# Optimization experiments

Measured on AMD Instinct MI355X. Metric: run time of the kernel, lower is better.

## Reference

```python
import jax, jax.numpy as jnp
import numpy as np

B, L, D = 16, 512, 128
EPS = 1e-12


def _newton_schulz_1(S):
    # One Newton-Schulz orthogonalization iteration on batched [B,D,D] matrices:
    # X = S/||S||_F ; X <- 1.5*X - 0.5 * X @ X^T @ X
    norm = jnp.sqrt(jnp.sum(S * S, axis=(-2, -1), keepdims=True)) + 1e-6
    X = S / norm
    XXtX = jnp.einsum('bij,bkj,bkl->bil', X, X, X)
    return 1.5 * X - 0.5 * XXtX


def _poly(v, coeffs):
    # PolynomialFeatureLayer, degree 2, dimension-preserving:
    # phi(v) = c0*v + c1*v^2
    return coeffs[0] * v + coeffs[1] * v * v


def setup_inputs() -> dict:
    key = jax.random.key(0)
    ks = jax.random.split(key, 6)
    s = 1.0 / np.sqrt(D)
    x = jax.random.normal(ks[0], (B, L, D), jnp.float32)
    Wq = jax.random.normal(ks[1], (D, D), jnp.float32) * s
    Wk = jax.random.normal(ks[2], (D, D), jnp.float32) * s
    Wout = jax.random.normal(ks[3], (D, D), jnp.float32) * s
    bout = jnp.zeros((D,), jnp.float32)
    M0 = jax.random.normal(ks[4], (D, D), jnp.float32) * 0.01   # M_init
    S0 = jnp.zeros((D, D), jnp.float32)                          # S_init
    P0 = jnp.eye(D, dtype=jnp.float32) * 0.01                    # P_init
    log_gain = jnp.zeros((D,), jnp.float32)                      # QKProjectionLayer gain
    coeffs = jnp.array([1.0, 0.5], jnp.float32)                  # poly coeffs
    return {"x": x, "Wq": Wq, "Wk": Wk, "P0": P0, "M0": M0, "S0": S0,
            "log_gain": log_gain, "coeffs": coeffs, "Wout": Wout, "bout": bout}


def reference(x, Wq, Wk, P0, M0, S0, log_gain, coeffs, Wout, bout):
    b, l, d = x.shape
    q = jnp.einsum('bld,ed->ble', x, Wq)                 # q_proj (no bias)
    k = jnp.einsum('bld,ed->ble', x, Wk)                 # k_proj (no bias)
    k = k / jnp.maximum(jnp.linalg.norm(k, axis=-1, keepdims=True), EPS)  # F.normalize

    # QKProjectionLayer: rotate q by per-batch projection P, tanh gate with learned gain
    P = jnp.broadcast_to(P0, (b, d, d))
    gain = jnp.exp(log_gain)
    q_aligned = jnp.tanh(gain * jnp.einsum('bld,bde->ble', q, P))
    # (P_new = 0.99*P + 0.01*mean_t outer(q,k); state only, unused by output)

    k_phi = _poly(k, coeffs)
    q_phi = _poly(q_aligned, coeffs)

    M = jnp.broadcast_to(M0, (b, d, d))
    S = jnpp = jnp.broadcast_to(S0, (b, d, d))

    def step(carry, inputs):
        M, S = carry
        k_t, q_t, x_t = inputs                           # each [B,D]
        pred = jnp.einsum('bde,be->bd', M, k_t)
        err = pred - x_t
        S = 0.9 * S + err[:, :, None] * k_t[:, None, :]  # outer-product grad
        S_ortho = _newton_schulz_1(S)
        M = 0.99 * M - 0.01 * S_ortho
        y_t = jnp.einsum('bde,be->bd', M, q_t)
        return (M, S), y_t

    xs = (jnp.swapaxes(k_phi, 0, 1), jnp.swapaxes(q_phi, 0, 1), jnp.swapaxes(x, 0, 1))
    (_, _), ys = jax.lax.scan(step, (M, S), xs)          # ys: [L,B,D]
    stacked = jnp.swapaxes(ys, 0, 1)                     # [B,L,D]
    out = jnp.einsum('bld,ed->ble', stacked, Wout) + bout  # out_proj
    return out
```

## Files before the change

### kernel.cpp

```cpp
#include <hip/hip_runtime.h>

#define BB 16
#define LL 512
#define DD 128
#define CH 16
#define NCH (LL / CH)

typedef float v2f __attribute__((ext_vector_type(2)));
__device__ __forceinline__ v2f mk2(float x, float y) { v2f r; r.x = x; r.y = y; return r; }
__device__ __forceinline__ v2f fma2(v2f a, v2f b, v2f c) {
    return __builtin_elementwise_fma(a, b, c);
}

__device__ __forceinline__ float red8(float v) {
    v += __int_as_float(__builtin_amdgcn_update_dpp(
            0, __float_as_int(v), 0xB1, 0xF, 0xF, true));
    v += __int_as_float(__builtin_amdgcn_update_dpp(
            0, __float_as_int(v), 0x4E, 0xF, 0xF, true));
    v += __int_as_float(__builtin_amdgcn_update_dpp(
            0, __float_as_int(v), 0x141, 0xF, 0xF, true));
    return v;
}

#define SCAN_REGS __attribute__((amdgpu_waves_per_eu(2, 2)))

__global__ void transpose3_kernel(const float* __restrict__ Wq,
                                  const float* __restrict__ Wk,
                                  const float* __restrict__ Wout,
                                  float* __restrict__ WqT,
                                  float* __restrict__ WkT,
                                  float* __restrict__ WoutT) {
    const float* src; float* dst;
    if (blockIdx.x == 0)      { src = Wq;   dst = WqT;   }
    else if (blockIdx.x == 1) { src = Wk;   dst = WkT;   }
    else                      { src = Wout; dst = WoutT; }
    for (int idx = threadIdx.x; idx < DD * DD; idx += blockDim.x) {
        int r = idx >> 7, c = idx & 127;
        dst[c * DD + r] = src[idx];
    }
}

__global__ __launch_bounds__(128) void prologue_kernel(
        const float* __restrict__ x, const float* __restrict__ WqT,
        const float* __restrict__ WkT, const float* __restrict__ P0,
        const float* __restrict__ log_gain, const float* __restrict__ coeffs,
        float* __restrict__ kphi, float* __restrict__ qphi) {
    const int row0 = blockIdx.x * 8;
    const int e = threadIdx.x;
    __shared__ float xs[8][DD];
    __shared__ float qrow[8][DD];
    __shared__ float wred[8][2];

    #pragma unroll
    for (int rr = 0; rr < 8; ++rr)
        xs[rr][e] = x[(size_t)(row0 + rr) * DD + e];
    __syncthreads();

    float aq[8] = {0,0,0,0,0,0,0,0}, ak[8] = {0,0,0,0,0,0,0,0};
    #pragma unroll 4
    for (int d = 0; d < DD; ++d) {
        float wq = WqT[d * DD + e];
        float wk = WkT[d * DD + e];
        #pragma unroll
        for (int rr = 0; rr < 8; ++rr) {
            float xv = xs[rr][d];
            aq[rr] = fmaf(xv, wq, aq[rr]);
            ak[rr] = fmaf(xv, wk, ak[rr]);
        }
    }
    const int lane = threadIdx.x & 63, wv = threadIdx.x >> 6;
    #pragma unroll
    for (int rr = 0; rr < 8; ++rr) {
        float s = ak[rr] * ak[rr];
        #pragma unroll
        for (int m = 1; m <= 32; m <<= 1) s += __shfl_xor(s, m);
        if (lane == 0) wred[rr][wv] = s;
    }
    __syncthreads();
    const float c0 = coeffs[0], c1v = coeffs[1];
    #pragma unroll
    for (int rr = 0; rr < 8; ++rr) {
        float s = wred[rr][0] + wred[rr][1];
        float kn = ak[rr] / fmaxf(sqrtf(s), 1e-12f);
        kphi[(size_t)(row0 + rr) * DD + e] = c0 * kn + c1v * kn * kn;
        qrow[rr][e] = aq[rr];
    }
    __syncthreads();
    float acc[8] = {0,0,0,0,0,0,0,0};
    #pragma unroll 4
    for (int d = 0; d < DD; ++d) {
        float pv = P0[d * DD + e];
        #pragma unroll
        for (int rr = 0; rr < 8; ++rr) acc[rr] = fmaf(qrow[rr][d], pv, acc[rr]);
    }
    const float g = expf(log_gain[e]);
    #pragma unroll
    for (int rr = 0; rr < 8; ++rr) {
        float qa = tanhf(g * acc[rr]);
        qphi[(size_t)(row0 + rr) * DD + e] = c0 * qa + c1v * qa * qa;
    }
}

__global__ SCAN_REGS __launch_bounds__(512)
void scan_kernel(
        const float* __restrict__ kphi, const float* __restrict__ qphi,
        const float* __restrict__ x, const float* __restrict__ M0,
        const float* __restrict__ S0, float* __restrict__ ys) {
    const int b    = blockIdx.x;
    const int tid  = threadIdx.x;
    const int j    = tid & 7;
    const int g    = tid >> 3;
    const int r0   = 2 * g;
    const int w    = tid >> 6;
    const int lane = tid & 63;

    __shared__ __align__(16) float kc[2][CH * DD];
    __shared__ __align__(16) float qc[2][CH * DD];
    __shared__ __align__(16) float xc[2][CH * DD];
    __shared__ __align__(16) float yc[CH * DD];
    __shared__ __align__(16) float us[DD], ps[DD], wsv[DD], hs[DD];
    __shared__ float red[64];
    __shared__ float n2sh;

    v2f S2[16], ST2[16], A2[16], M2[16];
    {
        const float4* S04 = (const float4*)S0;
        const float4* M04 = (const float4*)M0;
        #pragma unroll
        for (int rl = 0; rl < 2; ++rl)
            #pragma unroll
            for (int m = 0; m < 4; ++m) {
                int f4 = (r0 + rl) * 32 + j + 8 * m;
                float4 s4 = S04[f4], m4 = M04[f4];
                int p = rl * 8 + 2 * m;
                S2[p]     = mk2(s4.x, s4.y);
                S2[p + 1] = mk2(s4.z, s4.w);
                M2[p]     = mk2(m4.x, m4.y);
                M2[p + 1] = mk2(m4.z, m4.w);
            }
        #pragma unroll
        for (int rl = 0; rl < 2; ++rl)
            #pragma unroll
            for (int m = 0; m < 4; ++m) {
                int p = rl * 8 + 2 * m;
                ST2[p]     = mk2(S0[(size_t)(4*j + 32*m + 0) * DD + r0 + rl],
                                 S0[(size_t)(4*j + 32*m + 1) * DD + r0 + rl]);
                ST2[p + 1] = mk2(S0[(size_t)(4*j + 32*m + 2) * DD + r0 + rl],
                                 S0[(size_t)(4*j + 32*m + 3) * DD + r0 + rl]);
            }
        #pragma unroll
        for (int p = 0; p < 16; ++p) A2[p] = mk2(0.f, 0.f);
    }

    float sp = 0.f;
    #pragma unroll
    for (int p = 0; p < 16; ++p) {
        sp = fmaf(S2[p].x, S2[p].x, sp);
        sp = fmaf(S2[p].y, S2[p].y, sp);
    }
    sp = red8(sp);
    if (j == 0) red[g] = sp;

    const size_t base = (size_t)b * LL * DD;

    #pragma unroll
    for (int i = 0; i < 3; ++i) {
        int seg = w * 3 + i, arr = seg >> 3, sub = seg & 7;
        const float* sp0 = (arr == 0 ? kphi : (arr == 1 ? qphi : x))
                           + base + sub * 256 + lane * 4;
        float* dp = (arr == 0 ? kc[0] : (arr == 1 ? qc[0] : xc[0]))
                    + sub * 256 + lane * 4;
        *(float4*)dp = *(const float4*)sp0;
    }
    __syncthreads();
    if (tid < 64) {
        float s = red[tid];
        #pragma unroll
        for (int m = 1; m <= 32; m <<= 1) s += __shfl_xor(s, m);
        if (tid == 0) n2sh = s;
    }
    __syncthreads();
    float n2 = n2sh;

    const float a = 0.9f, a2v = 0.81f, a3v = 0.729f;
    const v2f av = mk2(a, a);

    v2f kk2[8];
    float u0, u1, p0, p1, cv;
    {
        const float4* k4 = (const float4*)kc[0];
        v2f pr0v = mk2(0.f, 0.f), pr1v = mk2(0.f, 0.f);
        v2f pp0v = mk2(0.f, 0.f), pp1v = mk2(0.f, 0.f);
        v2f cvv  = mk2(0.f, 0.f);
        #pragma unroll
        for (int m = 0; m < 4; ++m) {
            float4 v4 = k4[j + 8 * m];
            v2f k0 = mk2(v4.x, v4.y), k1 = mk2(v4.z, v4.w);
            kk2[2*m] = k0; kk2[2*m + 1] = k1;
            pr0v = fma2(M2[2*m],     k0, pr0v);
            pr0v = fma2(M2[2*m + 1], k1, pr0v);
            pr1v = fma2(M2[8 + 2*m],     k0, pr1v);
            pr1v = fma2(M2[8 + 2*m + 1], k1, pr1v);
            pp0v = fma2(S2[2*m],     k0, pp0v);
            pp0v = fma2(S2[2*m + 1], k1, pp0v);
            pp1v = fma2(S2[8 + 2*m],     k0, pp1v);
            pp1v = fma2(S2[8 + 2*m + 1], k1, pp1v);
            cvv  = fma2(k0, k0, cvv);
            cvv  = fma2(k1, k1, cvv);
        }
        float pr0 = red8(pr0v.x + pr0v.y);
        float pr1 = red8(pr1v.x + pr1v.y);
        p0 = red8(pp0v.x + pp0v.y);
        p1 = red8(pp1v.x + pp1v.y);
        cv = red8(cvv.x + cvv.y);
        const float2 xv = *(const float2*)&xc[0][r0];
        u0 = pr0 - xv.x; u1 = pr1 - xv.y;
        if (j == 0) {
            *(float2*)&us[r0] = make_float2(u0, u1);
            *(float2*)&ps[r0] = make_float2(p0, p1);
        }
    }
    __syncthreads();

    #pragma unroll 1
    for (int tc = 0; tc < NCH; ++tc) {
        const int cb = tc & 1;
        const float* kcb = kc[cb];
        const float* qcb = qc[cb];
        const float* xcb = xc[cb];

        #pragma unroll 1
        for (int sl = 0; sl < CH; ++sl) {
            const int so = sl * DD;
            const bool last = (tc == NCH - 1) && (sl == CH - 1);

            float4 pre0, pre1, pre2;
            const bool doPre = (sl == 0) && (tc + 1 < NCH);
            if (doPre) {
                const size_t nbg = base + (size_t)(tc + 1) * CH * DD;
                {
                    int seg = w * 3 + 0, arr = seg >> 3, sub = seg & 7;
                    pre0 = *(const float4*)((arr == 0 ? kphi : (arr == 1 ? qphi : x))
                                            + nbg + sub * 256 + lane * 4);
                }
                {
                    int seg = w * 3 + 1, arr = seg >> 3, sub = seg & 7;
                    pre1 = *(const float4*)((arr == 0 ? kphi : (arr == 1 ? qphi : x))
                                            + nbg + sub * 256 + lane * 4);
                }
                {
                    int seg = w * 3 + 2, arr = seg >> 3, sub = seg & 7;
                    pre2 = *(const float4*)((arr == 0 ? kphi : (arr == 1 ? qphi : x))
                                            + nbg + sub * 256 + lane * 4);
                }
            }

            v2f uu2[8], pa2[8];
            {
                const float4* u4 = (const float4*)us;
                const float4* p4 = (const float4*)ps;
                #pragma unroll
                for (int m = 0; m < 4; ++m) {
                    float4 a4 = u4[j + 8 * m], b4 = p4[j + 8 * m];
                    uu2[2*m]     = mk2(a4.x, a4.y);
                    uu2[2*m + 1] = mk2(a4.z, a4.w);
                    pa2[2*m]     = mk2(b4.x, b4.y);
                    pa2[2*m + 1] = mk2(b4.z, b4.w);
                }
            }
            const float2 vc = *(const float2*)&kcb[so + r0];
            const v2f vcx = mk2(vc.x, vc.x), vcy = mk2(vc.y, vc.y);
            v2f w0v = mk2(0.f, 0.f), w1v = mk2(0.f, 0.f);
            v2f h0v = mk2(0.f, 0.f), h1v = mk2(0.f, 0.f);
            v2f cuv = mk2(0.f, 0.f), cupv = mk2(0.f, 0.f);
            #pragma unroll
            for (int p = 0; p < 8; ++p) {
                v2f uv = uu2[p], pv = pa2[p];
                v2f st0 = ST2[p], st1 = ST2[8 + p];
                w0v  = fma2(st0, uv, w0v);
                w1v  = fma2(st1, uv, w1v);
                h0v  = fma2(st0, pv, h0v);
                h1v  = fma2(st1, pv, h1v);
                cuv  = fma2(uv, uv, cuv);
                cupv = fma2(uv, pv, cupv);
                ST2[p]     = fma2(av, st0, vcx * uv);
                ST2[8 + p] = fma2(av, st1, vcy * uv);
            }
            float w0 = red8(w0v.x + w0v.y);
            float w1 = red8(w1v.x + w1v.y);
            float h0 = red8(h0v.x + h0v.y);
            float h1 = red8(h1v.x + h1v.y);
            const float cu  = red8(cuv.x + cuv.y);
            const float cup = red8(cupv.x + cupv.y);
            n2 = a2v * n2 + 2.0f * a * cup + cu * cv;
            if (j == 0) {
                *(float2*)&wsv[r0] = make_float2(w0, w1);
                *(float2*)&hs[r0]  = make_float2(h0, h1);
            }
            if (doPre) {
                float* kn = kc[cb ^ 1]; float* qn = qc[cb ^ 1]; float* xn = xc[cb ^ 1];
                {
                    int seg = w * 3 + 0, arr = seg >> 3, sub = seg & 7;
                    *(float4*)((arr == 0 ? kn : (arr == 1 ? qn : xn))
                               + sub * 256 + lane * 4) = pre0;
                }
                {
                    int seg = w * 3 + 1, arr = seg >> 3, sub = seg & 7;
                    *(float4*)((arr == 0 ? kn : (arr == 1 ? qn : xn))
                               + sub * 256 + lane * 4) = pre1;
                }
                {
                    int seg = w * 3 + 2, arr = seg >> 3, sub = seg & 7;
                    *(float4*)((arr == 0 ? kn : (arr == 1 ? qn : xn))
                               + sub * 256 + lane * 4) = pre2;
                }
            }
            __syncthreads();

            v2f ww2[8];
            v2f g0v = mk2(0.f, 0.f), g1v = mk2(0.f, 0.f);
            {
                const float4* w4 = (const float4*)wsv;
                #pragma unroll
                for (int m = 0; m < 4; ++m) {
                    float4 a4 = w4[j + 8 * m];
                    v2f wv0 = mk2(a4.x, a4.y), wv1 = mk2(a4.z, a4.w);
                    ww2[2*m] = wv0; ww2[2*m + 1] = wv1;
                    g0v = fma2(S2[2*m],     wv0, g0v);
                    g0v = fma2(S2[2*m + 1], wv1, g0v);
                    g1v = fma2(S2[8 + 2*m],     wv0, g1v);
                    g1v = fma2(S2[8 + 2*m + 1], wv1, g1v);
                }
            }
            float g0 = red8(g0v.x + g0v.y);
            float g1 = red8(g1v.x + g1v.y);

            const float rho0 = a2v * g0 + a * cu * p0 + (a * cup + cv * cu) * u0;
            const float rho1 = a2v * g1 + a * cu * p1 + (a * cup + cv * cu) * u1;
            const float sg0  = a2v * p0 + a * cv * u0;
            const float sg1  = a2v * p1 + a * cv * u1;
            const float ta0  = a2v * u0, ta1 = a2v * u1;
            const float nrm  = sqrtf(fmaxf(n2, 0.f)) + 1e-6f;
            const float rn   = 1.0f / nrm;
            const float c1   = -0.015f * rn;
            const float c2   = 0.005f * rn * rn * rn;

            const v2f u0v = mk2(u0, u0),   u1v = mk2(u1, u1);
            const v2f r0v = mk2(rho0, rho0), r1v = mk2(rho1, rho1);
            const v2f s0v = mk2(sg0, sg0), s1v = mk2(sg1, sg1);
            const v2f t0v = mk2(ta0, ta0), t1v = mk2(ta1, ta1);
            const v2f a3p = mk2(a3v, a3v);
            const v2f c9p = mk2(0.99f, 0.99f);
            const v2f c1p = mk2(c1, c1), c2p = mk2(c2, c2);

            const float* knb = (sl + 1 < CH) ? (kcb + so + DD) : kc[cb ^ 1];
            const float* xnb = (sl + 1 < CH) ? (xcb + so + DD) : xc[cb ^ 1];

            v2f y0v = mk2(0.f, 0.f), y1v = mk2(0.f, 0.f);
            v2f pr0n = mk2(0.f, 0.f), pr1n = mk2(0.f, 0.f);
            v2f pp0n = mk2(0.f, 0.f), pp1n = mk2(0.f, 0.f);
            v2f cvn  = mk2(0.f, 0.f);
            v2f kkn[8];
            {
                const float4* h4  = (const float4*)hs;
                const float4* q4  = (const float4*)(qcb + so);
                const float4* k4n = (const float4*)knb;
                #pragma unroll
                for (int m = 0; m < 4; ++m) {
                    float4 b4  = h4[j + 8 * m];
                    float4 c4v = q4[j + 8 * m];
                    float4 k4v = k4n[j + 8 * m];
                    v2f hv0 = mk2(b4.x, b4.y),   hv1 = mk2(b4.z, b4.w);
                    v2f qv0 = mk2(c4v.x, c4v.y), qv1 = mk2(c4v.z, c4v.w);
                    v2f kn0 = mk2(k4v.x, k4v.y), kn1 = mk2(k4v.z, k4v.w);
                    kkn[2*m] = kn0; kkn[2*m + 1] = kn1;
                    v2f wv0 = ww2[2*m], wv1 = ww2[2*m + 1];
                    v2f kv0 = kk2[2*m], kv1 = kk2[2*m + 1];
                    v2f sn0 = fma2(av, S2[2*m],     u0v * kv0);
                    v2f sn1 = fma2(av, S2[2*m + 1], u0v * kv1);
                    S2[2*m] = sn0; S2[2*m + 1] = sn1;
                    v2f an0 = fma2(a3p, A2[2*m],
                                   fma2(r0v, kv0, fma2(s0v, wv0, t0v * hv0)));
                    v2f an1 = fma2(a3p, A2[2*m + 1],
                                   fma2(r0v, kv1, fma2(s0v, wv1, t0v * hv1)));
                    A2[2*m] = an0; A2[2*m + 1] = an1;
                    v2f mn0 = fma2(c9p, M2[2*m],     fma2(c1p, sn0, c2p * an0));
                    v2f mn1 = fma2(c9p, M2[2*m + 1], fma2(c1p, sn1, c2p * an1));
                    M2[2*m] = mn0; M2[2*m + 1] = mn1;
                    y0v  = fma2(mn0, qv0, y0v);
                    y0v  = fma2(mn1, qv1, y0v);
                    pr0n = fma2(mn0, kn0, pr0n);
                    pr0n = fma2(mn1, kn1, pr0n);
                    pp0n = fma2(sn0, kn0, pp0n);
                    pp0n = fma2(sn1, kn1, pp0n);
                    v2f sm0 = fma2(av, S2[8 + 2*m],     u1v * kv0);
                    v2f sm1 = fma2(av, S2[8 + 2*m + 1], u1v * kv1);
                    S2[8 + 2*m] = sm0; S2[8 + 2*m + 1] = sm1;
                    v2f am0 = fma2(a3p, A2[8 + 2*m],
                                   fma2(r1v, kv0, fma2(s1v, wv0, t1v * hv0)));
                    v2f am1 = fma2(a3p, A2[8 + 2*m + 1],
                                   fma2(r1v, kv1, fma2(s1v, wv1, t1v * hv1)));
                    A2[8 + 2*m] = am0; A2[8 + 2*m + 1] = am1;
                    v2f mm0 = fma2(c9p, M2[8 + 2*m],     fma2(c1p, sm0, c2p * am0));
                    v2f mm1 = fma2(c9p, M2[8 + 2*m + 1], fma2(c1p, sm1, c2p * am1));
                    M2[8 + 2*m] = mm0; M2[8 + 2*m + 1] = mm1;
                    y1v  = fma2(mm0, qv0, y1v);
                    y1v  = fma2(mm1, qv1, y1v);
                    pr1n = fma2(mm0, kn0, pr1n);
                    pr1n = fma2(mm1, kn1, pr1n);
                    pp1n = fma2(sm0, kn0, pp1n);
                    pp1n = fma2(sm1, kn1, pp1n);
                    cvn  = fma2(kn0, kn0, cvn);
                    cvn  = fma2(kn1, kn1, cvn);
                }
            }
            float y0 = red8(y0v.x + y0v.y);
            float y1 = red8(y1v.x + y1v.y);
            if (j == 0)
                *(float2*)&yc[so + r0] = make_float2(y0, y1);

            float pr0 = red8(pr0n.x + pr0n.y);
            float pr1 = red8(pr1n.x + pr1n.y);
            p0 = red8(pp0n.x + pp0n.y);
            p1 = red8(pp1n.x + pp1n.y);
            cv = red8(cvn.x + cvn.y);
            const float2 xn = *(const float2*)&xnb[r0];
            u0 = pr0 - xn.x; u1 = pr1 - xn.y;
            if (!last) {
                if (j == 0) {
                    *(float2*)&us[r0] = make_float2(u0, u1);
                    *(float2*)&ps[r0] = make_float2(p0, p1);
                }
                #pragma unroll
                for (int p = 0; p < 8; ++p) kk2[p] = kkn[p];
            }
            __syncthreads();
        }

        float4 yv = *(float4*)&yc[tid * 4];
        *(float4*)(ys + base + (size_t)tc * CH * DD + tid * 4) = yv;
    }
}

__global__ __launch_bounds__(128) void epilogue_kernel(
        const float* __restrict__ ys, const float* __restrict__ WoutT,
        const float* __restrict__ bout, float* __restrict__ out) {
    const int row0 = blockIdx.x * 8;
    const int e = threadIdx.x;
    __shared__ float yr[8][DD];
    #pragma unroll
    for (int rr = 0; rr < 8; ++rr)
        yr[rr][e] = ys[(size_t)(row0 + rr) * DD + e];
    __syncthreads();
    float acc[8] = {0,0,0,0,0,0,0,0};
    #pragma unroll 4
    for (int d = 0; d < DD; ++d) {
        float w = WoutT[d * DD + e];
        #pragma unroll
        for (int rr = 0; rr < 8; ++rr) acc[rr] = fmaf(yr[rr][d], w, acc[rr]);
    }
    const float bo = bout[e];
    #pragma unroll
    for (int rr = 0; rr < 8; ++rr)
        out[(size_t)(row0 + rr) * DD + e] = acc[rr] + bo;
}

extern "C" void kernel_launch(void* const* d_in, const int* in_sizes, int n_in,
                              void* d_out, int out_size, void* d_ws, size_t ws_size,
                              hipStream_t stream) {
    const float* x        = (const float*)d_in[0];
    const float* Wq       = (const float*)d_in[1];
    const float* Wk       = (const float*)d_in[2];
    const float* P0       = (const float*)d_in[3];
    const float* M0       = (const float*)d_in[4];
    const float* S0       = (const float*)d_in[5];
    const float* log_gain = (const float*)d_in[6];
    const float* coeffs   = (const float*)d_in[7];
    const float* Wout     = (const float*)d_in[8];
    const float* bout     = (const float*)d_in[9];
    float* out = (float*)d_out;

    float* ws    = (float*)d_ws;
    float* WqT   = ws;
    float* WkT   = ws + 16384;
    float* WoutT = ws + 32768;
    float* kphi  = ws + 49152;
    float* qphi  = kphi + (size_t)BB * LL * DD;
    float* ysb   = qphi + (size_t)BB * LL * DD;

    hipLaunchKernelGGL(transpose3_kernel, dim3(3), dim3(256), 0, stream,
                       Wq, Wk, Wout, WqT, WkT, WoutT);
    hipLaunchKernelGGL(prologue_kernel, dim3(BB * LL / 8), dim3(128), 0, stream,
                       x, WqT, WkT, P0, log_gain, coeffs, kphi, qphi);
    hipLaunchKernelGGL(scan_kernel, dim3(BB), dim3(512), 0, stream,
                       kphi, qphi, x, M0, S0, ysb);
    hipLaunchKernelGGL(epilogue_kernel, dim3(BB * LL / 8), dim3(128), 0, stream,
                       ysb, WoutT, bout, out);
}
```

Baseline: 1.172 ms.

## Fold per-step decay factors into chunk-local scaled state to cut multiplies

Rewrites the recurrences for S, S^T, A and M in a scaled frame whose decay factors (0.9, 0.729, 0.99) are held in a per-chunk step table in shared memory. Each inner step can then use pure FMA accumulations instead of separate scale-and-add. The state is renormalised by the accumulated decay powers at each chunk boundary. This removes a multiply per state element per step, at the cost of extra scalar rescales, a small table read each step, and possible loss of floating-point range or accuracy, since the scaled state grows by up to 0.729^-16 within a chunk.

Measured after the change: 1.115 ms. 4.8% less time.

```diff
diff --git a/kernel.cpp b/kernel.cpp
--- a/kernel.cpp
+++ b/kernel.cpp
@@ -119,8 +119,35 @@
     __shared__ __align__(16) float xc[2][CH * DD];
     __shared__ __align__(16) float yc[CH * DD];
     __shared__ __align__(16) float us[DD], ps[DD], wsv[DD], hs[DD];
+    __shared__ __align__(16) float ftab[CH][8];
     __shared__ float red[64];
     __shared__ float n2sh;
+
+    {
+        const float ia  = 1.0f / 0.9f;
+        const float ia3 = ia * ia * ia;
+        const float ra  = 0.9f / 0.99f;
+        const float ra3 = 0.729f / 0.99f;
+        float faS = 1.f, faiS = 1.f, fa3iS = 1.f;
+        float q1S = -0.015f, q3S = 0.005f, fmS = 1.f;
+        #pragma unroll 1
+        for (int s = 0; s < CH; ++s) {
+            float faN = faS * 0.9f;
+            faiS *= ia; fa3iS *= ia3; q1S *= ra; q3S *= ra3; fmS *= 0.99f;
+            if (tid == 0) {
+                ftab[s][0] = faS;   ftab[s][1] = faiS;
+                ftab[s][2] = faN;   ftab[s][3] = fa3iS;
+                ftab[s][4] = q1S;   ftab[s][5] = q3S;
+                ftab[s][6] = fmS;   ftab[s][7] = 0.f;
+            }
+            faS = faN;
+        }
+    }
+    const float a2c = 0.9f * 0.9f, a4c = a2c * a2c, a8c = a4c * a4c;
+    const float fa16 = a8c * a8c;
+    const float fa48 = fa16 * fa16 * fa16;
+    const float p2c = 0.99f * 0.99f, p4c = p2c * p2c, p8c = p4c * p4c;
+    const float pm16 = p8c * p8c;
 
     v2f S2[16], ST2[16], A2[16], M2[16];
     {
@@ -182,8 +209,7 @@
     __syncthreads();
     float n2 = n2sh;
 
-    const float a = 0.9f, a2v = 0.81f, a3v = 0.729f;
-    const v2f av = mk2(a, a);
+    const float a = 0.9f, a2v = 0.81f;
 
     v2f kk2[8];
     float u0, u1, p0, p1, cv;
@@ -234,6 +260,9 @@
             const int so = sl * DD;
             const bool last = (tc == NCH - 1) && (sl == CH - 1);
 
+            const float4 ft0 = *(const float4*)&ftab[sl][0];
+            const float4 ft1 = *(const float4*)&ftab[sl][4];
+
             float4 pre0, pre1, pre2;
             const bool doPre = (sl == 0) && (tc + 1 < NCH);
             if (doPre) {
@@ -269,7 +298,8 @@
                 }
             }
             const float2 vc = *(const float2*)&kcb[so + r0];
-            const v2f vcx = mk2(vc.x, vc.x), vcy = mk2(vc.y, vc.y);
+            const float vcxs = vc.x * ft0.y, vcys = vc.y * ft0.y;
+            const v2f vcx = mk2(vcxs, vcxs), vcy = mk2(vcys, vcys);
             v2f w0v = mk2(0.f, 0.f), w1v = mk2(0.f, 0.f);
             v2f h0v = mk2(0.f, 0.f), h1v = mk2(0.f, 0.f);
             v2f cuv = mk2(0.f, 0.f), cupv = mk2(0.f, 0.f);
@@ -283,13 +313,13 @@
                 h1v  = fma2(st1, pv, h1v);
                 cuv  = fma2(uv, uv, cuv);
                 cupv = fma2(uv, pv, cupv);
-                ST2[p]     = fma2(av, st0, vcx * uv);
-                ST2[8 + p] = fma2(av, st1, vcy * uv);
-            }
-            float w0 = red8(w0v.x + w0v.y);
-            float w1 = red8(w1v.x + w1v.y);
-            float h0 = red8(h0v.x + h0v.y);
-            float h1 = red8(h1v.x + h1v.y);
+                ST2[p]     = fma2(vcx, uv, st0);
+                ST2[8 + p] = fma2(vcy, uv, st1);
+            }
+            float w0 = red8(w0v.x + w0v.y) * ft0.x;
+            float w1 = red8(w1v.x + w1v.y) * ft0.x;
+            float h0 = red8(h0v.x + h0v.y) * ft0.x;
+            float h1 = red8(h1v.x + h1v.y) * ft0.x;
             const float cu  = red8(cuv.x + cuv.y);
             const float cup = red8(cupv.x + cupv.y);
             n2 = a2v * n2 + 2.0f * a * cup + cu * cv;
@@ -332,8 +362,8 @@
                     g1v = fma2(S2[8 + 2*m + 1], wv1, g1v);
                 }
             }
-            float g0 = red8(g0v.x + g0v.y);
-            float g1 = red8(g1v.x + g1v.y);
+            float g0 = red8(g0v.x + g0v.y) * ft0.x;
+            float g1 = red8(g1v.x + g1v.y) * ft0.x;
 
             const float rho0 = a2v * g0 + a * cu * p0 + (a * cup + cv * cu) * u0;
             const float rho1 = a2v * g1 + a * cu * p1 + (a * cup + cv * cu) * u1;
@@ -342,16 +372,20 @@
             const float ta0  = a2v * u0, ta1 = a2v * u1;
             const float nrm  = sqrtf(fmaxf(n2, 0.f)) + 1e-6f;
             const float rn   = 1.0f / nrm;
-            const float c1   = -0.015f * rn;
-            const float c2   = 0.005f * rn * rn * rn;
-
-            const v2f u0v = mk2(u0, u0),   u1v = mk2(u1, u1);
-            const v2f r0v = mk2(rho0, rho0), r1v = mk2(rho1, rho1);
-            const v2f s0v = mk2(sg0, sg0), s1v = mk2(sg1, sg1);
-            const v2f t0v = mk2(ta0, ta0), t1v = mk2(ta1, ta1);
-            const v2f a3p = mk2(a3v, a3v);
-            const v2f c9p = mk2(0.99f, 0.99f);
-            const v2f c1p = mk2(c1, c1), c2p = mk2(c2, c2);
+            const float rn3  = rn * rn * rn;
+            const float c1s  = rn * ft1.x;
+            const float c2s  = rn3 * ft1.y;
+            const float f3i  = ft0.w;
+            const float u0p  = u0 * ft0.y, u1p = u1 * ft0.y;
+
+            const v2f u0v = mk2(u0p, u0p), u1v = mk2(u1p, u1p);
+            const v2f r0v = mk2(rho0 * f3i, rho0 * f3i);
+            const v2f r1v = mk2(rho1 * f3i, rho1 * f3i);
+            const v2f s0v = mk2(sg0 * f3i, sg0 * f3i);
+            const v2f s1v = mk2(sg1 * f3i, sg1 * f3i);
+            const v2f t0v = mk2(ta0 * f3i, ta0 * f3i);
+            const v2f t1v = mk2(ta1 * f3i, ta1 * f3i);
+            const v2f c1p = mk2(c1s, c1s), c2p = mk2(c2s, c2s);
 
             const float* knb = (sl + 1 < CH) ? (kcb + so + DD) : kc[cb ^ 1];
             const float* xnb = (sl + 1 < CH) ? (xcb + so + DD) : xc[cb ^ 1];
@@ -376,16 +410,14 @@
                     kkn[2*m] = kn0; kkn[2*m + 1] = kn1;
                     v2f wv0 = ww2[2*m], wv1 = ww2[2*m + 1];
                     v2f kv0 = kk2[2*m], kv1 = kk2[2*m + 1];
-                    v2f sn0 = fma2(av, S2[2*m],     u0v * kv0);
-                    v2f sn1 = fma2(av, S2[2*m + 1], u0v * kv1);
+                    v2f sn0 = fma2(u0v, kv0, S2[2*m]);
+                    v2f sn1 = fma2(u0v, kv1, S2[2*m + 1]);
                     S2[2*m] = sn0; S2[2*m + 1] = sn1;
-                    v2f an0 = fma2(a3p, A2[2*m],
-                                   fma2(r0v, kv0, fma2(s0v, wv0, t0v * hv0)));
-                    v2f an1 = fma2(a3p, A2[2*m + 1],
-                                   fma2(r0v, kv1, fma2(s0v, wv1, t0v * hv1)));
+                    v2f an0 = fma2(r0v, kv0, fma2(s0v, wv0, fma2(t0v, hv0, A2[2*m])));
+                    v2f an1 = fma2(r0v, kv1, fma2(s0v, wv1, fma2(t0v, hv1, A2[2*m + 1])));
                     A2[2*m] = an0; A2[2*m + 1] = an1;
-                    v2f mn0 = fma2(c9p, M2[2*m],     fma2(c1p, sn0, c2p * an0));
-                    v2f mn1 = fma2(c9p, M2[2*m + 1], fma2(c1p, sn1, c2p * an1));
+                    v2f mn0 = fma2(c1p, sn0, fma2(c2p, an0, M2[2*m]));
+                    v2f mn1 = fma2(c1p, sn1, fma2(c2p, an1, M2[2*m + 1]));
                     M2[2*m] = mn0; M2[2*m + 1] = mn1;
                     y0v  = fma2(mn0, qv0, y0v);
                     y0v  = fma2(mn1, qv1, y0v);
@@ -393,16 +425,14 @@
                     pr0n = fma2(mn1, kn1, pr0n);
                     pp0n = fma2(sn0, kn0, pp0n);
                     pp0n = fma2(sn1, kn1, pp0n);
-                    v2f sm0 = fma2(av, S2[8 + 2*m],     u1v * kv0);
-                    v2f sm1 = fma2(av, S2[8 + 2*m + 1], u1v * kv1);
+                    v2f sm0 = fma2(u1v, kv0, S2[8 + 2*m]);
+                    v2f sm1 = fma2(u1v, kv1, S2[8 + 2*m + 1]);
                     S2[8 + 2*m] = sm0; S2[8 + 2*m + 1] = sm1;
-                    v2f am0 = fma2(a3p, A2[8 + 2*m],
-                                   fma2(r1v, kv0, fma2(s1v, wv0, t1v * hv0)));
-                    v2f am1 = fma2(a3p, A2[8 + 2*m + 1],
-                                   fma2(r1v, kv1, fma2(s1v, wv1, t1v * hv1)));
+                    v2f am0 = fma2(r1v, kv0, fma2(s1v, wv0, fma2(t1v, hv0, A2[8 + 2*m])));
+                    v2f am1 = fma2(r1v, kv1, fma2(s1v, wv1, fma2(t1v, hv1, A2[8 + 2*m + 1])));
                     A2[8 + 2*m] = am0; A2[8 + 2*m + 1] = am1;
-                    v2f mm0 = fma2(c9p, M2[8 + 2*m],     fma2(c1p, sm0, c2p * am0));
-                    v2f mm1 = fma2(c9p, M2[8 + 2*m + 1], fma2(c1p, sm1, c2p * am1));
+                    v2f mm0 = fma2(c1p, sm0, fma2(c2p, am0, M2[8 + 2*m]));
+                    v2f mm1 = fma2(c1p, sm1, fma2(c2p, am1, M2[8 + 2*m + 1]));
                     M2[8 + 2*m] = mm0; M2[8 + 2*m + 1] = mm1;
                     y1v  = fma2(mm0, qv0, y1v);
                     y1v  = fma2(mm1, qv1, y1v);
@@ -414,15 +444,15 @@
                     cvn  = fma2(kn1, kn1, cvn);
                 }
             }
-            float y0 = red8(y0v.x + y0v.y);
-            float y1 = red8(y1v.x + y1v.y);
+            float y0 = red8(y0v.x + y0v.y) * ft1.z;
+            float y1 = red8(y1v.x + y1v.y) * ft1.z;
             if (j == 0)
                 *(float2*)&yc[so + r0] = make_float2(y0, y1);
 
-            float pr0 = red8(pr0n.x + pr0n.y);
-            float pr1 = red8(pr1n.x + pr1n.y);
-            p0 = red8(pp0n.x + pp0n.y);
-            p1 = red8(pp1n.x + pp1n.y);
+            float pr0 = red8(pr0n.x + pr0n.y) * ft1.z;
+            float pr1 = red8(pr1n.x + pr1n.y) * ft1.z;
+            p0 = red8(pp0n.x + pp0n.y) * ft0.z;
+            p1 = red8(pp1n.x + pp1n.y) * ft0.z;
             cv = red8(cvn.x + cvn.y);
             const float2 xn = *(const float2*)&xnb[r0];
             u0 = pr0 - xn.x; u1 = pr1 - xn.y;
@@ -439,6 +469,16 @@
 
         float4 yv = *(float4*)&yc[tid * 4];
         *(float4*)(ys + base + (size_t)tc * CH * DD + tid * 4) = yv;
+
+        if (tc + 1 < NCH) {
+            const v2f rs = mk2(fa16, fa16);
+            const v2f rA = mk2(fa48, fa48);
+            const v2f rM = mk2(pm16, pm16);
+            #pragma unroll
+            for (int p = 0; p < 16; ++p) {
+                S2[p] *= rs; ST2[p] *= rs; A2[p] *= rA; M2[p] *= rM;
+            }
+        }
     }
 }
 
```
